# Kernel tuning notes

Measured on AMD Instinct MI355X. Metric: run time of the kernel, lower is better.

## Reference

```python
import jax, jax.numpy as jnp
import numpy as np

B = 32768          # batch (replay-buffer minibatch)
OBS, ACT = 17, 6   # HalfCheetah-style dims
IN = OBS + ACT
H = 256            # hidden width hard-coded in the module
N = 10             # num_q_nets


def setup_inputs() -> dict:
    key = jax.random.key(0)
    ks = jax.random.split(key, 8)
    # PyTorch Linear default init: U(-1/sqrt(fan_in), 1/sqrt(fan_in)); scale randn similarly.
    s1, s2, s3 = 1.0 / np.sqrt(IN), 1.0 / np.sqrt(H), 1.0 / np.sqrt(H)
    return {
        "state": jax.random.normal(ks[0], (B, OBS), dtype=jnp.float32),
        "action": jax.random.uniform(ks[1], (B, ACT), dtype=jnp.float32, minval=-1.0, maxval=1.0),
        "W1": jax.random.normal(ks[2], (N, IN, H), dtype=jnp.float32) * s1,
        "b1": jax.random.normal(ks[3], (N, H), dtype=jnp.float32) * s1,
        "W2": jax.random.normal(ks[4], (N, H, H), dtype=jnp.float32) * s2,
        "b2": jax.random.normal(ks[5], (N, H), dtype=jnp.float32) * s2,
        "W3": jax.random.normal(ks[6], (N, H, 1), dtype=jnp.float32) * s3,
        "b3": jax.random.normal(ks[7], (N, 1), dtype=jnp.float32) * s3,
    }


def reference(state, action, W1, b1, W2, b2, W3, b3):
    # x: [B, OBS+ACT]
    x = jnp.concatenate([state, action], axis=1)
    # batched-over-ensemble GEMMs; n=ensemble member, b=batch
    h1 = jax.nn.relu(jnp.einsum("bi,nih->nbh", x, W1) + b1[:, None, :])   # [N,B,H]
    h2 = jax.nn.relu(jnp.einsum("nbh,nho->nbo", h1, W2) + b2[:, None, :])  # [N,B,H]
    out = jnp.einsum("nbh,nho->nbo", h2, W3) + b3[:, None, :]              # [N,B,1]
    return out
```

## Files before the change

### kernel.cpp

```cpp
#include <hip/hip_runtime.h>
#include <hip/hip_bf16.h>


typedef __attribute__((ext_vector_type(8))) short bf16x8;
typedef __attribute__((ext_vector_type(4))) float f32x4;

#define B_TOTAL 32768
#define NQ 10
#define HDIM 256
#define BT 128

#define XP_ELEMS  (B_TOTAL * 32)
#define W1P_ELEMS (NQ * 16 * 64 * 8)
#define W2P_ELEMS (NQ * 8 * 16 * 64 * 8)

__device__ __forceinline__ unsigned short f2bf(float f) {
  unsigned int u = __float_as_uint(f);
  u = u + 0x7FFFu + ((u >> 16) & 1u);
  return (unsigned short)(u >> 16);
}

__device__ __forceinline__ unsigned int pk2bf(float a, float b) {
  union { __hip_bfloat162 h; unsigned int u; } cv;
  cv.h = __float22bfloat162_rn(make_float2(a, b));
  return cv.u;
}

__global__ void pack_all_kernel(const float* __restrict__ state,
                                const float* __restrict__ action,
                                const float* __restrict__ W1,
                                const float* __restrict__ W2,
                                unsigned short* __restrict__ xp,
                                unsigned short* __restrict__ w1p,
                                unsigned short* __restrict__ w2p) {
  int t = blockIdx.x * 256 + threadIdx.x;
  const int NX  = B_TOTAL * 4;
  const int NW1 = NQ * 16 * 64;
  if (t < NX) {
    int b = t >> 2, seg = t & 3;
    unsigned short v[8];
    if (seg < 2) {
      const float* sp = state + (size_t)b * 17 + seg * 8;
#pragma unroll
      for (int j = 0; j < 8; j++) v[j] = f2bf(sp[j]);
    } else if (seg == 2) {
      v[0] = f2bf(state[(size_t)b * 17 + 16]);
#pragma unroll
      for (int j = 0; j < 6; j++) v[1 + j] = f2bf(action[(size_t)b * 6 + j]);
      v[7] = 0;
    } else {
#pragma unroll
      for (int j = 0; j < 8; j++) v[j] = 0;
    }
    *(uint4*)&xp[(size_t)t * 8] = *(const uint4*)v;
  } else if (t < NX + NW1) {
    int u = t - NX;
    int lane = u & 63, mt = (u >> 6) & 15, n = u >> 10;
    int m = lane & 15, q = lane >> 4;
    int outc = mt * 16 + m;
    unsigned short v[8];
#pragma unroll
    for (int j = 0; j < 8; j++) {
      int k = q * 8 + j;
      v[j] = (k < 23) ? f2bf(W1[(n * 23 + k) * 256 + outc]) : (unsigned short)0;
    }
    *(uint4*)&w1p[(size_t)u * 8] = *(const uint4*)v;
  } else {
    int u = t - NX - NW1;
    int lane = u & 63, mt = (u >> 6) & 15, kt = (u >> 10) & 7, n = u >> 13;
    int m = lane & 15, q = lane >> 4;
    int outc = mt * 16 + m;
    unsigned short v[8];
#pragma unroll
    for (int j = 0; j < 8; j++) {
      int h = kt * 32 + q * 8 + j;
      v[j] = f2bf(W2[((size_t)(n * 256 + h)) * 256 + outc]);
    }
    *(uint4*)&w2p[(size_t)u * 8] = *(const uint4*)v;
  }
}

__global__ __launch_bounds__(512, 4) void fused_ensemble_kernel(
    const unsigned short* __restrict__ xp,
    const unsigned short* __restrict__ w1p,
    const float* __restrict__ b1,
    const unsigned short* __restrict__ w2p,
    const float* __restrict__ b2,
    const float* __restrict__ W3,
    const float* __restrict__ b3,
    float* __restrict__ out) {
  __shared__ __align__(16) unsigned short hs[32 * BT * 8];
  __shared__ float red[8 * 64];

  const int tid = threadIdx.x;
  const int lane = tid & 63;
  const int w = tid >> 6;
  const int m = lane & 15;
  const int q = lane >> 4;
  const int cg = w >> 1;
  const int colg = w & 1;

  const int n = blockIdx.x >> 8;
  const int row0 = (blockIdx.x & 255) * BT;

  f32x4 acc[4][4];

  {
    bf16x8 af[4], bfr[4];
#pragma unroll
    for (int nt = 0; nt < 4; nt++) {
      int col = row0 + colg * 64 + nt * 16 + m;
      bfr[nt] = *(const bf16x8*)(xp + (size_t)col * 32 + q * 8);
    }
#pragma unroll
    for (int mt = 0; mt < 4; mt++)
      af[mt] = *(const bf16x8*)(w1p + (((size_t)n * 16 + cg * 4 + mt) * 64 + lane) * 8);
#pragma unroll
    for (int mt = 0; mt < 4; mt++) {
      float4 bv = *(const float4*)&b1[n * HDIM + (cg * 4 + mt) * 16 + q * 4];
      f32x4 bi = (f32x4){bv.x, bv.y, bv.z, bv.w};
#pragma unroll
      for (int nt = 0; nt < 4; nt++) acc[mt][nt] = bi;
    }
#pragma unroll
    for (int nt = 0; nt < 4; nt++)
#pragma unroll
      for (int mt = 0; mt < 4; mt++)
        acc[mt][nt] = __builtin_amdgcn_mfma_f32_16x16x32_bf16(af[mt], bfr[nt], acc[mt][nt], 0, 0, 0);
  }

#pragma unroll
  for (int mt = 0; mt < 4; mt++) {
    int kq = cg * 8 + mt * 2 + (q >> 1);
    int joff = (q & 1) * 4;
#pragma unroll
    for (int nt = 0; nt < 4; nt++) {
      int col = colg * 64 + nt * 16 + m;
      f32x4 a = acc[mt][nt];
      uint2 wv;
      wv.x = pk2bf(fmaxf(a[0], 0.f), fmaxf(a[1], 0.f));
      wv.y = pk2bf(fmaxf(a[2], 0.f), fmaxf(a[3], 0.f));
      *(uint2*)&hs[((size_t)kq * BT + col) * 8 + joff] = wv;
    }
  }
  __syncthreads();

  {
    const unsigned short* w2n = w2p + (size_t)n * (8 * 16 * 64 * 8);
    bf16x8 acur[4], anxt[4];
#pragma unroll
    for (int mt = 0; mt < 4; mt++)
      acur[mt] = *(const bf16x8*)(w2n + (((size_t)cg * 4 + mt) * 64 + lane) * 8);
#pragma unroll
    for (int mt = 0; mt < 4; mt++) {
      float4 bv = *(const float4*)&b2[n * HDIM + (cg * 4 + mt) * 16 + q * 4];
      f32x4 bi = (f32x4){bv.x, bv.y, bv.z, bv.w};
#pragma unroll
      for (int nt = 0; nt < 4; nt++) acc[mt][nt] = bi;
    }
#pragma unroll
    for (int kt = 0; kt < 8; kt++) {
      if (kt < 7) {
#pragma unroll
        for (int mt = 0; mt < 4; mt++)
          anxt[mt] = *(const bf16x8*)(w2n + (((size_t)(kt + 1) * 16 + cg * 4 + mt) * 64 + lane) * 8);
      }
      bf16x8 bfr[4];
#pragma unroll
      for (int nt = 0; nt < 4; nt++)
        bfr[nt] = *(const bf16x8*)&hs[(((size_t)kt * 4 + q) * BT + colg * 64 + nt * 16 + m) * 8];
#pragma unroll
      for (int nt = 0; nt < 4; nt++)
#pragma unroll
        for (int mt = 0; mt < 4; mt++)
          acc[mt][nt] = __builtin_amdgcn_mfma_f32_16x16x32_bf16(acur[mt], bfr[nt], acc[mt][nt], 0, 0, 0);
#pragma unroll
      for (int mt = 0; mt < 4; mt++) acur[mt] = anxt[mt];
    }
  }

  {
    float4 w3v[4];
#pragma unroll
    for (int mt = 0; mt < 4; mt++)
      w3v[mt] = *(const float4*)&W3[n * HDIM + (cg * 4 + mt) * 16 + q * 4];
    float p[4];
#pragma unroll
    for (int nt = 0; nt < 4; nt++) {
      float s = 0.f;
#pragma unroll
      for (int mt = 0; mt < 4; mt++) {
        f32x4 a = acc[mt][nt];
        float4 wv = w3v[mt];
        s = fmaf(fmaxf(a[0], 0.f), wv.x, s);
        s = fmaf(fmaxf(a[1], 0.f), wv.y, s);
        s = fmaf(fmaxf(a[2], 0.f), wv.z, s);
        s = fmaf(fmaxf(a[3], 0.f), wv.w, s);
      }
      s += __shfl_xor(s, 16, 64);
      s += __shfl_xor(s, 32, 64);
      p[nt] = s;
    }
    if (q == 0) {
#pragma unroll
      for (int nt = 0; nt < 4; nt++) red[w * 64 + nt * 16 + m] = p[nt];
    }
    __syncthreads();
    if (tid < BT) {
      int g = tid >> 6, lc = tid & 63;
      float s = b3[n];
#pragma unroll
      for (int c = 0; c < 4; c++) s += red[(c * 2 + g) * 64 + lc];
      out[(size_t)n * B_TOTAL + row0 + tid] = s;
    }
  }
}

extern "C" void kernel_launch(void* const* d_in, const int* in_sizes, int n_in,
                              void* d_out, int out_size, void* d_ws, size_t ws_size,
                              hipStream_t stream) {
  const float* state  = (const float*)d_in[0];
  const float* action = (const float*)d_in[1];
  const float* W1 = (const float*)d_in[2];
  const float* b1 = (const float*)d_in[3];
  const float* W2 = (const float*)d_in[4];
  const float* b2 = (const float*)d_in[5];
  const float* W3 = (const float*)d_in[6];
  const float* b3 = (const float*)d_in[7];
  float* out = (float*)d_out;

  unsigned short* xp  = (unsigned short*)d_ws;
  unsigned short* w1p = (unsigned short*)((char*)d_ws + (size_t)XP_ELEMS * 2);
  unsigned short* w2p = (unsigned short*)((char*)d_ws + (size_t)(XP_ELEMS + W1P_ELEMS) * 2);

  pack_all_kernel<<<872, 256, 0, stream>>>(state, action, W1, W2, xp, w1p, w2p);
  fused_ensemble_kernel<<<NQ * (B_TOTAL / BT), 512, 0, stream>>>(
      xp, w1p, b1, w2p, b2, W3, b3, out);
}
```

Baseline: 118.7 us.

## Switch layer-2 GEMM to 32x32x16 MFMA with repacked W2 and prefetched LDS operands

Layer 2 now uses the 32x32x16 bf16 MFMA instead of 16x16x32. W2 is repacked to match the new fragment layout, and the LDS B-operand loads are double-buffered alongside the weight prefetch. The W2 prefetch and the b2 bias init are hoisted before the layer-1 epilogue. The larger MFMA tile is meant to cut instruction count and LDS reads per FLOP. In exchange it uses 16-wide accumulators, which may raise register pressure and lower occupancy.

```diff
diff --git a/kernel.cpp b/kernel.cpp
--- a/kernel.cpp
+++ b/kernel.cpp
@@ -4,6 +4,7 @@
 
 typedef __attribute__((ext_vector_type(8))) short bf16x8;
 typedef __attribute__((ext_vector_type(4))) float f32x4;
+typedef __attribute__((ext_vector_type(16))) float f32x16;
 
 #define B_TOTAL 32768
 #define NQ 10
@@ -12,7 +13,7 @@
 
 #define XP_ELEMS  (B_TOTAL * 32)
 #define W1P_ELEMS (NQ * 16 * 64 * 8)
-#define W2P_ELEMS (NQ * 8 * 16 * 64 * 8)
+#define W2P_ELEMS (NQ * 16 * 8 * 64 * 8)
 
 __device__ __forceinline__ unsigned short f2bf(float f) {
   unsigned int u = __float_as_uint(f);
@@ -67,14 +68,14 @@
     *(uint4*)&w1p[(size_t)u * 8] = *(const uint4*)v;
   } else {
     int u = t - NX - NW1;
-    int lane = u & 63, mt = (u >> 6) & 15, kt = (u >> 10) & 7, n = u >> 13;
-    int m = lane & 15, q = lane >> 4;
-    int outc = mt * 16 + m;
+    int lane = u & 63, mt = (u >> 6) & 7, kt = (u >> 9) & 15, n = u >> 13;
+    int l31 = lane & 31, lh = lane >> 5;
+    int ch = mt * 32 + l31;
     unsigned short v[8];
 #pragma unroll
     for (int j = 0; j < 8; j++) {
-      int h = kt * 32 + q * 8 + j;
-      v[j] = f2bf(W2[((size_t)(n * 256 + h)) * 256 + outc]);
+      int k = kt * 16 + lh * 8 + j;
+      v[j] = f2bf(W2[((size_t)(n * 256 + k)) * 256 + ch]);
     }
     *(uint4*)&w2p[(size_t)u * 8] = *(const uint4*)v;
   }
@@ -97,14 +98,17 @@
   const int w = tid >> 6;
   const int m = lane & 15;
   const int q = lane >> 4;
+  const int l31 = lane & 31;
+  const int lh = lane >> 5;
   const int cg = w >> 1;
   const int colg = w & 1;
 
   const int n = blockIdx.x >> 8;
   const int row0 = (blockIdx.x & 255) * BT;
 
+  const unsigned short* w2n = w2p + (size_t)n * (16 * 8 * 64 * 8);
+
   f32x4 acc[4][4];
-
   {
     bf16x8 af[4], bfr[4];
 #pragma unroll
@@ -127,6 +131,28 @@
 #pragma unroll
       for (int mt = 0; mt < 4; mt++)
         acc[mt][nt] = __builtin_amdgcn_mfma_f32_16x16x32_bf16(af[mt], bfr[nt], acc[mt][nt], 0, 0, 0);
+  }
+
+  bf16x8 acur[2], anxt[2], bcur[2], bnxt[2];
+#pragma unroll
+  for (int mt = 0; mt < 2; mt++)
+    acur[mt] = *(const bf16x8*)(w2n + (((size_t)0 * 8 + cg * 2 + mt) * 64 + lane) * 8);
+
+  f32x16 acc2[2][2];
+#pragma unroll
+  for (int mt = 0; mt < 2; mt++) {
+    int chb = n * HDIM + cg * 64 + mt * 32 + 4 * lh;
+    float4 bv0 = *(const float4*)&b2[chb + 0];
+    float4 bv1 = *(const float4*)&b2[chb + 8];
+    float4 bv2 = *(const float4*)&b2[chb + 16];
+    float4 bv3 = *(const float4*)&b2[chb + 24];
+    f32x16 bi;
+    bi[0] = bv0.x; bi[1] = bv0.y; bi[2] = bv0.z; bi[3] = bv0.w;
+    bi[4] = bv1.x; bi[5] = bv1.y; bi[6] = bv1.z; bi[7] = bv1.w;
+    bi[8] = bv2.x; bi[9] = bv2.y; bi[10] = bv2.z; bi[11] = bv2.w;
+    bi[12] = bv3.x; bi[13] = bv3.y; bi[14] = bv3.z; bi[15] = bv3.w;
+    acc2[mt][0] = bi;
+    acc2[mt][1] = bi;
   }
 
 #pragma unroll
@@ -146,64 +172,63 @@
   __syncthreads();
 
   {
-    const unsigned short* w2n = w2p + (size_t)n * (8 * 16 * 64 * 8);
-    bf16x8 acur[4], anxt[4];
-#pragma unroll
-    for (int mt = 0; mt < 4; mt++)
-      acur[mt] = *(const bf16x8*)(w2n + (((size_t)cg * 4 + mt) * 64 + lane) * 8);
-#pragma unroll
-    for (int mt = 0; mt < 4; mt++) {
-      float4 bv = *(const float4*)&b2[n * HDIM + (cg * 4 + mt) * 16 + q * 4];
-      f32x4 bi = (f32x4){bv.x, bv.y, bv.z, bv.w};
-#pragma unroll
-      for (int nt = 0; nt < 4; nt++) acc[mt][nt] = bi;
-    }
-#pragma unroll
-    for (int kt = 0; kt < 8; kt++) {
-      if (kt < 7) {
-#pragma unroll
-        for (int mt = 0; mt < 4; mt++)
-          anxt[mt] = *(const bf16x8*)(w2n + (((size_t)(kt + 1) * 16 + cg * 4 + mt) * 64 + lane) * 8);
+#pragma unroll
+    for (int nt = 0; nt < 2; nt++)
+      bcur[nt] = *(const bf16x8*)&hs[(((size_t)0 * 2 + lh) * BT + colg * 64 + nt * 32 + l31) * 8];
+#pragma unroll
+    for (int kt = 0; kt < 16; kt++) {
+      if (kt < 15) {
+#pragma unroll
+        for (int mt = 0; mt < 2; mt++)
+          anxt[mt] = *(const bf16x8*)(w2n + (((size_t)(kt + 1) * 8 + cg * 2 + mt) * 64 + lane) * 8);
+#pragma unroll
+        for (int nt = 0; nt < 2; nt++)
+          bnxt[nt] = *(const bf16x8*)&hs[(((size_t)(kt + 1) * 2 + lh) * BT + colg * 64 + nt * 32 + l31) * 8];
       }
-      bf16x8 bfr[4];
-#pragma unroll
-      for (int nt = 0; nt < 4; nt++)
-        bfr[nt] = *(const bf16x8*)&hs[(((size_t)kt * 4 + q) * BT + colg * 64 + nt * 16 + m) * 8];
-#pragma unroll
-      for (int nt = 0; nt < 4; nt++)
-#pragma unroll
-        for (int mt = 0; mt < 4; mt++)
-          acc[mt][nt] = __builtin_amdgcn_mfma_f32_16x16x32_bf16(acur[mt], bfr[nt], acc[mt][nt], 0, 0, 0);
-#pragma unroll
-      for (int mt = 0; mt < 4; mt++) acur[mt] = anxt[mt];
+#pragma unroll
+      for (int nt = 0; nt < 2; nt++)
+#pragma unroll
+        for (int mt = 0; mt < 2; mt++)
+          acc2[mt][nt] = __builtin_amdgcn_mfma_f32_32x32x16_bf16(acur[mt], bcur[nt], acc2[mt][nt], 0, 0, 0);
+      if (kt < 15) {
+#pragma unroll
+        for (int mt = 0; mt < 2; mt++) acur[mt] = anxt[mt];
+#pragma unroll
+        for (int nt = 0; nt < 2; nt++) bcur[nt] = bnxt[nt];
+      }
     }
   }
 
   {
-    float4 w3v[4];
-#pragma unroll
-    for (int mt = 0; mt < 4; mt++)
-      w3v[mt] = *(const float4*)&W3[n * HDIM + (cg * 4 + mt) * 16 + q * 4];
-    float p[4];
-#pragma unroll
-    for (int nt = 0; nt < 4; nt++) {
+    float4 w3v[2][4];
+#pragma unroll
+    for (int mt = 0; mt < 2; mt++) {
+      int chb = n * HDIM + cg * 64 + mt * 32 + 4 * lh;
+      w3v[mt][0] = *(const float4*)&W3[chb + 0];
+      w3v[mt][1] = *(const float4*)&W3[chb + 8];
+      w3v[mt][2] = *(const float4*)&W3[chb + 16];
+      w3v[mt][3] = *(const float4*)&W3[chb + 24];
+    }
+    float p[2];
+#pragma unroll
+    for (int nt = 0; nt < 2; nt++) {
       float s = 0.f;
 #pragma unroll
-      for (int mt = 0; mt < 4; mt++) {
-        f32x4 a = acc[mt][nt];
-        float4 wv = w3v[mt];
-        s = fmaf(fmaxf(a[0], 0.f), wv.x, s);
-        s = fmaf(fmaxf(a[1], 0.f), wv.y, s);
-        s = fmaf(fmaxf(a[2], 0.f), wv.z, s);
-        s = fmaf(fmaxf(a[3], 0.f), wv.w, s);
-      }
-      s += __shfl_xor(s, 16, 64);
+      for (int mt = 0; mt < 2; mt++)
+#pragma unroll
+        for (int g = 0; g < 4; g++) {
+          const float4 wv = w3v[mt][g];
+          s = fmaf(fmaxf(acc2[mt][nt][g * 4 + 0], 0.f), wv.x, s);
+          s = fmaf(fmaxf(acc2[mt][nt][g * 4 + 1], 0.f), wv.y, s);
+          s = fmaf(fmaxf(acc2[mt][nt][g * 4 + 2], 0.f), wv.z, s);
+          s = fmaf(fmaxf(acc2[mt][nt][g * 4 + 3], 0.f), wv.w, s);
+        }
       s += __shfl_xor(s, 32, 64);
       p[nt] = s;
     }
-    if (q == 0) {
-#pragma unroll
-      for (int nt = 0; nt < 4; nt++) red[w * 64 + nt * 16 + m] = p[nt];
+    if (lh == 0) {
+#pragma unroll
+      for (int nt = 0; nt < 2; nt++) red[w * 64 + nt * 32 + l31] = p[nt];
     }
     __syncthreads();
     if (tid < BT) {
```

After: 123.6 us. 4.1% more time.
